# Performance work log

Measured on AMD Instinct MI355X. Metric: run time of the kernel, lower is better.

Reference implementation:

```python
import jax, jax.numpy as jnp
import numpy as np

NEG_SLOPE = 0.01  # torch F.leaky_relu default


def _mlp_block(x, mask, W, b):
    # x: [B,P,V,F]; mask: [B,P,V] bool; W: [H,F]; b: [H]
    h = jax.nn.leaky_relu(jnp.einsum('bpvf,hf->bpvh', x, W) + b, NEG_SLOPE)
    m = mask[..., None]
    out = jnp.where(m, h, 0.0)                                   # zeros at masked-out slots
    neg = jnp.where(m, out, -jnp.inf)
    pool = jnp.max(neg, axis=2, keepdims=True)                   # [B,P,1,H] masked max-pool
    any_valid = jnp.any(mask, axis=2)[:, :, None, None]
    pool = jnp.where(any_valid, pool, 0.0)                       # fully-masked polylines -> 0
    rep = jnp.broadcast_to(pool, out.shape)
    return jnp.concatenate([out, rep], axis=-1)                  # [B,P,V,2H]


def setup_inputs() -> dict:
    key = jax.random.key(0)
    ks = jax.random.split(key, 8)
    B, P, V, F, H = 32, 512, 32, 16, 64
    input_var = jax.random.normal(ks[0], (B, P, V, F), dtype=jnp.float32)
    input_mask = jax.random.bernoulli(ks[1], 0.8, (B, P, V))
    s = 1.0 / np.sqrt(F)
    W1 = jax.random.uniform(ks[2], (H, F), jnp.float32, -s, s)
    b1 = jax.random.uniform(ks[3], (H,), jnp.float32, -s, s)
    s2 = 1.0 / np.sqrt(2 * H)
    W2 = jax.random.uniform(ks[4], (H, 2 * H), jnp.float32, -s2, s2)
    b2 = jax.random.uniform(ks[5], (H,), jnp.float32, -s2, s2)
    W3 = jax.random.uniform(ks[6], (H, 2 * H), jnp.float32, -s2, s2)
    b3 = jax.random.uniform(ks[7], (H,), jnp.float32, -s2, s2)
    return {"input_var": input_var, "input_mask": input_mask,
            "W1": W1, "b1": b1, "W2": W2, "b2": b2, "W3": W3, "b3": b3,
            "size1": P, "size2": V}


def reference(input_var, input_mask, W1, b1, W2, b2, W3, b3, size1, size2):
    hidden = W1.shape[0]
    x = _mlp_block(input_var, input_mask, W1, b1)
    y = _mlp_block(x, input_mask, W2, b2)
    z = _mlp_block(y, input_mask, W3, b3)
    out = z[:, :, 0, -hidden:]                                   # pooled half, same across V
    out = jnp.where(jnp.any(input_mask, axis=2)[..., None], out, 0.0)
    return out
```

## Files before the change

kernel.cpp:

```cpp
#include <hip/hip_runtime.h>
#include <math.h>

namespace {
constexpr int kXS = 72;
constexpr float kSlope = 0.01f;

typedef short bf16x8 __attribute__((ext_vector_type(8)));
typedef float f32x4  __attribute__((ext_vector_type(4)));
typedef float f32x4v __attribute__((ext_vector_type(4)));
typedef int   i32x4v __attribute__((ext_vector_type(4)));

__device__ __forceinline__ float lrelu(float x) { return fmaxf(x, kSlope * x); }

__device__ __forceinline__ unsigned short bfrne(float a) {
    union { float f; unsigned u; } v; v.f = a;
    return (unsigned short)((v.u + 0x7FFFu + ((v.u >> 16) & 1u)) >> 16);
}

__device__ __forceinline__ short2 cvtpk(float a, float b) {
#if __has_builtin(__builtin_amdgcn_cvt_pk_bf16_f32)
    auto p = __builtin_amdgcn_cvt_pk_bf16_f32(a, b);
    short2 s; __builtin_memcpy(&s, &p, sizeof(s)); return s;
#else
    short2 s; s.x = (short)bfrne(a); s.y = (short)bfrne(b); return s;
#endif
}
__device__ __forceinline__ int cvtpk_i(float a, float b) {
    short2 s = cvtpk(a, b);
    int r; __builtin_memcpy(&r, &s, sizeof(r)); return r;
}

__global__ void prep_weights(const float* __restrict__ W1,
                             const float* __restrict__ W2,
                             const float* __restrict__ W3,
                             unsigned short* __restrict__ ws)
{
    int t = blockIdx.x * blockDim.x + threadIdx.x;
    if (t >= 36 * 64) return;
    int f = t >> 6, l = t & 63, c = l & 15, q = l >> 4;
    unsigned short v[8] = {0, 0, 0, 0, 0, 0, 0, 0};
    const float* src = nullptr; int row = 0, k0 = 0, K = 0;
    if (f < 4) {
        if (q < 2) { src = W1; row = 16 * f + c; k0 = q * 8; K = 16; }
    } else if (f < 20) {
        int g = f - 4;  src = W2; row = 16 * (g >> 2) + c; k0 = (g & 3) * 32 + q * 8; K = 128;
    } else {
        int g = f - 20; src = W3; row = 16 * (g >> 2) + c; k0 = (g & 3) * 32 + q * 8; K = 128;
    }
    if (src) {
        #pragma unroll
        for (int j = 0; j < 8; ++j) v[j] = bfrne(src[row * K + k0 + j]);
    }
    unsigned short* dst = ws + (size_t)f * 512 + l * 8;
    *(ushort4*)(dst)     = make_ushort4(v[0], v[1], v[2], v[3]);
    *(ushort4*)(dst + 4) = make_ushort4(v[4], v[5], v[6], v[7]);
}

__global__ __launch_bounds__(128, 6) void fused_mlp_v9(
    const float* __restrict__ X, const int* __restrict__ M,
    const unsigned short* __restrict__ WF,
    const float* __restrict__ B1, const float* __restrict__ B2,
    const float* __restrict__ B3, float* __restrict__ OUT)
{
    __shared__ __align__(16) short xb[32 * kXS];
    __shared__ __align__(16) short pl[64];

    const int t = threadIdx.x, u = t >> 6, l = t & 63, c = l & 15, q = l >> 4;
    const size_t bp = (size_t)blockIdx.x;
    const int nb = 32 * u;

    f32x4v xr[2][2];
    if (q < 2) {
        #pragma unroll
        for (int mt = 0; mt < 2; ++mt) {
            const f32x4v* p = (const f32x4v*)(X + (bp * 32 + 16 * mt + c) * 16 + q * 8);
            xr[mt][0] = __builtin_nontemporal_load(p);
            xr[mt][1] = __builtin_nontemporal_load(p + 1);
        }
    }
    const i32x4v* Mp = (const i32x4v*)(M + bp * 32);
    const i32x4v mr0 = __builtin_nontemporal_load(Mp + q);
    const i32x4v mr1 = __builtin_nontemporal_load(Mp + 4 + q);
    const unsigned mbits =
        (mr0[0] ? 1u : 0u)  | (mr0[1] ? 2u : 0u)  | (mr0[2] ? 4u : 0u)  | (mr0[3] ? 8u : 0u) |
        (mr1[0] ? 16u : 0u) | (mr1[1] ? 32u : 0u) | (mr1[2] ? 64u : 0u) | (mr1[3] ? 128u : 0u);
    const bool anyv = __any(mbits != 0);

    float mz[8], mn[8];
    #pragma unroll
    for (int i = 0; i < 8; ++i) {
        bool mk = (mbits >> i) & 1;
        mz[i] = mk ? 1.f : 0.f;
        mn[i] = mk ? 0.f : -INFINITY;
    }

    f32x4 acc[2][2];

    {
        bf16x8 a1f[2];
        #pragma unroll
        for (int mt = 0; mt < 2; ++mt) {
            union { bf16x8 v; int i[4]; } uu;
            uu.v = bf16x8{};
            if (q < 2) {
                f32x4v f0 = xr[mt][0], f1 = xr[mt][1];
                uu.i[0] = cvtpk_i(f0[0], f0[1]);
                uu.i[1] = cvtpk_i(f0[2], f0[3]);
                uu.i[2] = cvtpk_i(f1[0], f1[1]);
                uu.i[3] = cvtpk_i(f1[2], f1[3]);
            }
            a1f[mt] = uu.v;
        }
        #pragma unroll
        for (int nt = 0; nt < 2; ++nt) {
            float b = B1[nb + 16 * nt + c];
            bf16x8 wf = *(const bf16x8*)(WF + (size_t)(2 * u + nt) * 512 + l * 8);
            f32x4 c0 = { b, b, b, b };
            acc[0][nt] = __builtin_amdgcn_mfma_f32_16x16x32_bf16(a1f[0], wf, c0, 0, 0, 0);
            acc[1][nt] = __builtin_amdgcn_mfma_f32_16x16x32_bf16(a1f[1], wf, c0, 0, 0, 0);
        }
    }

    auto epilogue = [&]() {
        float pool[2];
        #pragma unroll
        for (int nt = 0; nt < 2; ++nt) {
            float pv = -INFINITY;
            #pragma unroll
            for (int mt = 0; mt < 2; ++mt) {
                short* base = &xb[(16 * mt + 4 * q) * kXS + nb + 16 * nt + c];
                float o[4];
                #pragma unroll
                for (int r = 0; r < 4; ++r) {
                    float y = lrelu(acc[mt][nt][r]);
                    o[r] = y * mz[mt * 4 + r];
                    pv = fmaxf(pv, y + mn[mt * 4 + r]);
                }
                short2 s01 = cvtpk(o[0], o[1]);
                short2 s23 = cvtpk(o[2], o[3]);
                base[0 * kXS] = s01.x; base[1 * kXS] = s01.y;
                base[2 * kXS] = s23.x; base[3 * kXS] = s23.y;
            }
            pv = fmaxf(pv, __shfl_xor(pv, 16));
            pv = fmaxf(pv, __shfl_xor(pv, 32));
            pool[nt] = anyv ? pv : 0.f;
        }
        if (q < 2) pl[nb + 16 * q + c] = (short)bfrne(q ? pool[1] : pool[0]);
    };

    auto layerK = [&](int fb, const float* __restrict__ Bv) {
        bf16x8 a00 = *(const bf16x8*)&xb[(     c) * kXS      + q * 8];
        bf16x8 a01 = *(const bf16x8*)&xb[(16 + c) * kXS      + q * 8];
        bf16x8 a10 = *(const bf16x8*)&xb[(     c) * kXS + 32 + q * 8];
        bf16x8 a11 = *(const bf16x8*)&xb[(16 + c) * kXS + 32 + q * 8];
        bf16x8 ap0 = *(const bf16x8*)&pl[q * 8];
        bf16x8 ap1 = *(const bf16x8*)&pl[32 + q * 8];
        #pragma unroll
        for (int nt = 0; nt < 2; ++nt) {
            float b = Bv[nb + 16 * nt + c];
            acc[0][nt] = f32x4{ b, b, b, b };
            acc[1][nt] = acc[0][nt];
        }
        #pragma unroll
        for (int ks = 0; ks < 4; ++ks) {
            bf16x8 am0 = (ks == 0) ? a00 : (ks == 1) ? a10 : (ks == 2) ? ap0 : ap1;
            bf16x8 am1 = (ks == 0) ? a01 : (ks == 1) ? a11 : (ks == 2) ? ap0 : ap1;
            #pragma unroll
            for (int nt = 0; nt < 2; ++nt) {
                int f = fb + (2 * u + nt) * 4 + ks;
                bf16x8 wf = *(const bf16x8*)(WF + (size_t)f * 512 + l * 8);
                acc[0][nt] = __builtin_amdgcn_mfma_f32_16x16x32_bf16(am0, wf, acc[0][nt], 0, 0, 0);
                acc[1][nt] = __builtin_amdgcn_mfma_f32_16x16x32_bf16(am1, wf, acc[1][nt], 0, 0, 0);
            }
        }
    };

    epilogue();
    __syncthreads();
    layerK(4, B2);
    __syncthreads();
    epilogue();
    __syncthreads();
    layerK(20, B3);

    #pragma unroll
    for (int nt = 0; nt < 2; ++nt) {
        float pv = -INFINITY;
        #pragma unroll
        for (int mt = 0; mt < 2; ++mt)
            #pragma unroll
            for (int r = 0; r < 4; ++r) {
                float y = lrelu(acc[mt][nt][r]);
                pv = fmaxf(pv, y + mn[mt * 4 + r]);
            }
        pv = fmaxf(pv, __shfl_xor(pv, 16));
        pv = fmaxf(pv, __shfl_xor(pv, 32));
        pv = anyv ? pv : 0.f;
        if (q == 0) __builtin_nontemporal_store(pv, &OUT[bp * 64 + nb + 16 * nt + c]);
    }
}
}

extern "C" void kernel_launch(void* const* d_in, const int* in_sizes, int n_in,
                              void* d_out, int out_size, void* d_ws, size_t ws_size,
                              hipStream_t stream) {
    (void)in_sizes; (void)n_in; (void)ws_size; (void)out_size;
    const float* X  = (const float*)d_in[0];
    const int*   M  = (const int*)d_in[1];
    const float* W1 = (const float*)d_in[2];
    const float* B1 = (const float*)d_in[3];
    const float* W2 = (const float*)d_in[4];
    const float* B2 = (const float*)d_in[5];
    const float* W3 = (const float*)d_in[6];
    const float* B3 = (const float*)d_in[7];
    float* OUT = (float*)d_out;
    unsigned short* WF = (unsigned short*)d_ws;

    prep_weights<<<(36 * 64 + 255) / 256, 256, 0, stream>>>(W1, W2, W3, WF);
    fused_mlp_v9<<<16384, 128, 0, stream>>>(X, M, WF, B1, B2, B3, OUT);
}
```

Measured before the change: 130.9 us.

## Make kernel persistent with register-resident weights and prefetch of next polyline

Launches 2048 blocks that each loop over 8 polylines instead of one block per polyline. All layer weights and biases are loaded into registers once per block, and the next polyline's inputs and mask are prefetched while the current one is computed. Shared buffers are double-buffered by iteration parity. The extra registers lower the occupancy hint from 6 to 3 blocks per SIMD, so there is less latency hiding from other waves, and load balance is coarser.

```diff
diff --git a/kernel.cpp b/kernel.cpp
--- a/kernel.cpp
+++ b/kernel.cpp
@@ -16,7 +16,6 @@
     union { float f; unsigned u; } v; v.f = a;
     return (unsigned short)((v.u + 0x7FFFu + ((v.u >> 16) & 1u)) >> 16);
 }
-
 __device__ __forceinline__ short2 cvtpk(float a, float b) {
 #if __has_builtin(__builtin_amdgcn_cvt_pk_bf16_f32)
     auto p = __builtin_amdgcn_cvt_pk_bf16_f32(a, b);
@@ -56,47 +55,73 @@
     *(ushort4*)(dst + 4) = make_ushort4(v[4], v[5], v[6], v[7]);
 }
 
-__global__ __launch_bounds__(128, 6) void fused_mlp_v9(
+__global__ __launch_bounds__(128, 3) void fused_mlp_v10(
     const float* __restrict__ X, const int* __restrict__ M,
     const unsigned short* __restrict__ WF,
     const float* __restrict__ B1, const float* __restrict__ B2,
     const float* __restrict__ B3, float* __restrict__ OUT)
 {
-    __shared__ __align__(16) short xb[32 * kXS];
-    __shared__ __align__(16) short pl[64];
+    __shared__ __align__(16) short xb[2][32 * kXS];
+    __shared__ __align__(16) short pl[2][64];
 
     const int t = threadIdx.x, u = t >> 6, l = t & 63, c = l & 15, q = l >> 4;
-    const size_t bp = (size_t)blockIdx.x;
     const int nb = 32 * u;
 
+    bf16x8 w1f[2], w2f[2][4], w3f[2][4];
+    #pragma unroll
+    for (int nt = 0; nt < 2; ++nt) {
+        const int ng = 2 * u + nt;
+        w1f[nt] = *(const bf16x8*)(WF + (size_t)ng * 512 + l * 8);
+        #pragma unroll
+        for (int ks = 0; ks < 4; ++ks) {
+            w2f[nt][ks] = *(const bf16x8*)(WF + (size_t)(4 + ng * 4 + ks) * 512 + l * 8);
+            w3f[nt][ks] = *(const bf16x8*)(WF + (size_t)(20 + ng * 4 + ks) * 512 + l * 8);
+        }
+    }
+    float b1[2], b2[2], b3[2];
+    #pragma unroll
+    for (int nt = 0; nt < 2; ++nt) {
+        b1[nt] = B1[nb + 16 * nt + c];
+        b2[nt] = B2[nb + 16 * nt + c];
+        b3[nt] = B3[nb + 16 * nt + c];
+    }
+
+    size_t bp = (size_t)blockIdx.x;
     f32x4v xr[2][2];
-    if (q < 2) {
-        #pragma unroll
-        for (int mt = 0; mt < 2; ++mt) {
-            const f32x4v* p = (const f32x4v*)(X + (bp * 32 + 16 * mt + c) * 16 + q * 8);
-            xr[mt][0] = __builtin_nontemporal_load(p);
-            xr[mt][1] = __builtin_nontemporal_load(p + 1);
-        }
-    }
-    const i32x4v* Mp = (const i32x4v*)(M + bp * 32);
-    const i32x4v mr0 = __builtin_nontemporal_load(Mp + q);
-    const i32x4v mr1 = __builtin_nontemporal_load(Mp + 4 + q);
-    const unsigned mbits =
-        (mr0[0] ? 1u : 0u)  | (mr0[1] ? 2u : 0u)  | (mr0[2] ? 4u : 0u)  | (mr0[3] ? 8u : 0u) |
-        (mr1[0] ? 16u : 0u) | (mr1[1] ? 32u : 0u) | (mr1[2] ? 64u : 0u) | (mr1[3] ? 128u : 0u);
-    const bool anyv = __any(mbits != 0);
-
-    float mz[8], mn[8];
-    #pragma unroll
-    for (int i = 0; i < 8; ++i) {
-        bool mk = (mbits >> i) & 1;
-        mz[i] = mk ? 1.f : 0.f;
-        mn[i] = mk ? 0.f : -INFINITY;
+    i32x4v mr0, mr1;
+    {
+        if (q < 2) {
+            #pragma unroll
+            for (int mt = 0; mt < 2; ++mt) {
+                const f32x4v* p = (const f32x4v*)(X + (bp * 32 + 16 * mt + c) * 16 + q * 8);
+                xr[mt][0] = __builtin_nontemporal_load(p);
+                xr[mt][1] = __builtin_nontemporal_load(p + 1);
+            }
+        }
+        const i32x4v* Mp = (const i32x4v*)(M + bp * 32);
+        mr0 = __builtin_nontemporal_load(Mp + q);
+        mr1 = __builtin_nontemporal_load(Mp + 4 + q);
     }
 
     f32x4 acc[2][2];
 
-    {
+    #pragma unroll 1
+    for (int it = 0; it < 8; ++it) {
+        const size_t bp_cur = bp;
+        short* xbc = &xb[it & 1][0];
+        short* plc = &pl[it & 1][0];
+
+        const unsigned mbits =
+            (mr0[0] ? 1u : 0u)  | (mr0[1] ? 2u : 0u)  | (mr0[2] ? 4u : 0u)  | (mr0[3] ? 8u : 0u) |
+            (mr1[0] ? 16u : 0u) | (mr1[1] ? 32u : 0u) | (mr1[2] ? 64u : 0u) | (mr1[3] ? 128u : 0u);
+        const bool anyv = __any(mbits != 0);
+        float mz[8], mn[8];
+        #pragma unroll
+        for (int i = 0; i < 8; ++i) {
+            bool mk = (mbits >> i) & 1;
+            mz[i] = mk ? 1.f : 0.f;
+            mn[i] = mk ? 0.f : -INFINITY;
+        }
         bf16x8 a1f[2];
         #pragma unroll
         for (int mt = 0; mt < 2; ++mt) {
@@ -111,92 +136,103 @@
             }
             a1f[mt] = uu.v;
         }
+
+        if (it < 7) {
+            bp += 2048;
+            if (q < 2) {
+                #pragma unroll
+                for (int mt = 0; mt < 2; ++mt) {
+                    const f32x4v* p = (const f32x4v*)(X + (bp * 32 + 16 * mt + c) * 16 + q * 8);
+                    xr[mt][0] = __builtin_nontemporal_load(p);
+                    xr[mt][1] = __builtin_nontemporal_load(p + 1);
+                }
+            }
+            const i32x4v* Mp = (const i32x4v*)(M + bp * 32);
+            mr0 = __builtin_nontemporal_load(Mp + q);
+            mr1 = __builtin_nontemporal_load(Mp + 4 + q);
+        }
+
         #pragma unroll
         for (int nt = 0; nt < 2; ++nt) {
-            float b = B1[nb + 16 * nt + c];
-            bf16x8 wf = *(const bf16x8*)(WF + (size_t)(2 * u + nt) * 512 + l * 8);
-            f32x4 c0 = { b, b, b, b };
-            acc[0][nt] = __builtin_amdgcn_mfma_f32_16x16x32_bf16(a1f[0], wf, c0, 0, 0, 0);
-            acc[1][nt] = __builtin_amdgcn_mfma_f32_16x16x32_bf16(a1f[1], wf, c0, 0, 0, 0);
-        }
-    }
-
-    auto epilogue = [&]() {
-        float pool[2];
+            f32x4 c0 = { b1[nt], b1[nt], b1[nt], b1[nt] };
+            acc[0][nt] = __builtin_amdgcn_mfma_f32_16x16x32_bf16(a1f[0], w1f[nt], c0, 0, 0, 0);
+            acc[1][nt] = __builtin_amdgcn_mfma_f32_16x16x32_bf16(a1f[1], w1f[nt], c0, 0, 0, 0);
+        }
+
+        auto epilogue = [&]() {
+            float pool[2];
+            #pragma unroll
+            for (int nt = 0; nt < 2; ++nt) {
+                float pv = -INFINITY;
+                #pragma unroll
+                for (int mt = 0; mt < 2; ++mt) {
+                    short* base = &xbc[(16 * mt + 4 * q) * kXS + nb + 16 * nt + c];
+                    float o[4];
+                    #pragma unroll
+                    for (int r = 0; r < 4; ++r) {
+                        float y = lrelu(acc[mt][nt][r]);
+                        o[r] = y * mz[mt * 4 + r];
+                        pv = fmaxf(pv, y + mn[mt * 4 + r]);
+                    }
+                    short2 s01 = cvtpk(o[0], o[1]);
+                    short2 s23 = cvtpk(o[2], o[3]);
+                    base[0 * kXS] = s01.x; base[1 * kXS] = s01.y;
+                    base[2 * kXS] = s23.x; base[3 * kXS] = s23.y;
+                }
+                pv = fmaxf(pv, __shfl_xor(pv, 16));
+                pv = fmaxf(pv, __shfl_xor(pv, 32));
+                pool[nt] = anyv ? pv : 0.f;
+            }
+            if (q < 2) plc[nb + 16 * q + c] = (short)bfrne(q ? pool[1] : pool[0]);
+        };
+
+        auto layerK = [&](const bf16x8 (&wf)[2][4], const float (&bv)[2]) {
+            bf16x8 a00 = *(const bf16x8*)&xbc[(     c) * kXS      + q * 8];
+            bf16x8 a01 = *(const bf16x8*)&xbc[(16 + c) * kXS      + q * 8];
+            bf16x8 a10 = *(const bf16x8*)&xbc[(     c) * kXS + 32 + q * 8];
+            bf16x8 a11 = *(const bf16x8*)&xbc[(16 + c) * kXS + 32 + q * 8];
+            bf16x8 ap0 = *(const bf16x8*)&plc[q * 8];
+            bf16x8 ap1 = *(const bf16x8*)&plc[32 + q * 8];
+            #pragma unroll
+            for (int nt = 0; nt < 2; ++nt) {
+                acc[0][nt] = f32x4{ bv[nt], bv[nt], bv[nt], bv[nt] };
+                acc[1][nt] = acc[0][nt];
+            }
+            #pragma unroll
+            for (int ks = 0; ks < 4; ++ks) {
+                bf16x8 am0 = (ks == 0) ? a00 : (ks == 1) ? a10 : (ks == 2) ? ap0 : ap1;
+                bf16x8 am1 = (ks == 0) ? a01 : (ks == 1) ? a11 : (ks == 2) ? ap0 : ap1;
+                #pragma unroll
+                for (int nt = 0; nt < 2; ++nt) {
+                    acc[0][nt] = __builtin_amdgcn_mfma_f32_16x16x32_bf16(am0, wf[nt][ks], acc[0][nt], 0, 0, 0);
+                    acc[1][nt] = __builtin_amdgcn_mfma_f32_16x16x32_bf16(am1, wf[nt][ks], acc[1][nt], 0, 0, 0);
+                }
+            }
+        };
+
+        epilogue();
+        __syncthreads();
+        layerK(w2f, b2);
+        __syncthreads();
+        epilogue();
+        __syncthreads();
+        layerK(w3f, b3);
+
         #pragma unroll
         for (int nt = 0; nt < 2; ++nt) {
             float pv = -INFINITY;
             #pragma unroll
-            for (int mt = 0; mt < 2; ++mt) {
-                short* base = &xb[(16 * mt + 4 * q) * kXS + nb + 16 * nt + c];
-                float o[4];
+            for (int mt = 0; mt < 2; ++mt)
                 #pragma unroll
                 for (int r = 0; r < 4; ++r) {
                     float y = lrelu(acc[mt][nt][r]);
-                    o[r] = y * mz[mt * 4 + r];
                     pv = fmaxf(pv, y + mn[mt * 4 + r]);
                 }
-                short2 s01 = cvtpk(o[0], o[1]);
-                short2 s23 = cvtpk(o[2], o[3]);
-                base[0 * kXS] = s01.x; base[1 * kXS] = s01.y;
-                base[2 * kXS] = s23.x; base[3 * kXS] = s23.y;
-            }
             pv = fmaxf(pv, __shfl_xor(pv, 16));
             pv = fmaxf(pv, __shfl_xor(pv, 32));
-            pool[nt] = anyv ? pv : 0.f;
-        }
-        if (q < 2) pl[nb + 16 * q + c] = (short)bfrne(q ? pool[1] : pool[0]);
-    };
-
-    auto layerK = [&](int fb, const float* __restrict__ Bv) {
-        bf16x8 a00 = *(const bf16x8*)&xb[(     c) * kXS      + q * 8];
-        bf16x8 a01 = *(const bf16x8*)&xb[(16 + c) * kXS      + q * 8];
-        bf16x8 a10 = *(const bf16x8*)&xb[(     c) * kXS + 32 + q * 8];
-        bf16x8 a11 = *(const bf16x8*)&xb[(16 + c) * kXS + 32 + q * 8];
-        bf16x8 ap0 = *(const bf16x8*)&pl[q * 8];
-        bf16x8 ap1 = *(const bf16x8*)&pl[32 + q * 8];
-        #pragma unroll
-        for (int nt = 0; nt < 2; ++nt) {
-            float b = Bv[nb + 16 * nt + c];
-            acc[0][nt] = f32x4{ b, b, b, b };
-            acc[1][nt] = acc[0][nt];
-        }
-        #pragma unroll
-        for (int ks = 0; ks < 4; ++ks) {
-            bf16x8 am0 = (ks == 0) ? a00 : (ks == 1) ? a10 : (ks == 2) ? ap0 : ap1;
-            bf16x8 am1 = (ks == 0) ? a01 : (ks == 1) ? a11 : (ks == 2) ? ap0 : ap1;
-            #pragma unroll
-            for (int nt = 0; nt < 2; ++nt) {
-                int f = fb + (2 * u + nt) * 4 + ks;
-                bf16x8 wf = *(const bf16x8*)(WF + (size_t)f * 512 + l * 8);
-                acc[0][nt] = __builtin_amdgcn_mfma_f32_16x16x32_bf16(am0, wf, acc[0][nt], 0, 0, 0);
-                acc[1][nt] = __builtin_amdgcn_mfma_f32_16x16x32_bf16(am1, wf, acc[1][nt], 0, 0, 0);
-            }
-        }
-    };
-
-    epilogue();
-    __syncthreads();
-    layerK(4, B2);
-    __syncthreads();
-    epilogue();
-    __syncthreads();
-    layerK(20, B3);
-
-    #pragma unroll
-    for (int nt = 0; nt < 2; ++nt) {
-        float pv = -INFINITY;
-        #pragma unroll
-        for (int mt = 0; mt < 2; ++mt)
-            #pragma unroll
-            for (int r = 0; r < 4; ++r) {
-                float y = lrelu(acc[mt][nt][r]);
-                pv = fmaxf(pv, y + mn[mt * 4 + r]);
-            }
-        pv = fmaxf(pv, __shfl_xor(pv, 16));
-        pv = fmaxf(pv, __shfl_xor(pv, 32));
-        pv = anyv ? pv : 0.f;
-        if (q == 0) __builtin_nontemporal_store(pv, &OUT[bp * 64 + nb + 16 * nt + c]);
+            pv = anyv ? pv : 0.f;
+            if (q == 0) __builtin_nontemporal_store(pv, &OUT[bp_cur * 64 + nb + 16 * nt + c]);
+        }
     }
 }
 }
@@ -217,5 +253,5 @@
     unsigned short* WF = (unsigned short*)d_ws;
 
     prep_weights<<<(36 * 64 + 255) / 256, 256, 0, stream>>>(W1, W2, W3, WF);
-    fused_mlp_v9<<<16384, 128, 0, stream>>>(X, M, WF, B1, B2, B3, OUT);
-}
+    fused_mlp_v10<<<2048, 128, 0, stream>>>(X, M, WF, B1, B2, B3, OUT);
+}
```

Measured after the change: 165.9 us. 26.7% more time.
